# Kernel optimization log

Measured on AMD Instinct MI355X. Metric: run time of the kernel, lower is better.

The kernel has to match this reference:

```python
import jax, jax.numpy as jnp
import numpy as np

EPS = 1e-7  # K.epsilon()
SR = 10.0


def setup_inputs() -> dict:
    key = jax.random.key(0)
    ks = jax.random.split(key, 6)
    B, T, D, U = 32, 1024, 512, 64
    x1 = jax.random.normal(ks[0], (B, T, D), jnp.float32)
    x2 = jax.random.normal(ks[1], (B, T, D), jnp.float32)
    w1 = jax.random.normal(ks[2], (D, U), jnp.float32) * (2.0 / (D + U)) ** 0.5
    w2 = jax.random.normal(ks[3], (T, U), jnp.float32) * (2.0 / (T + U)) ** 0.5
    w3 = jax.random.normal(ks[4], (T, U), jnp.float32) * (2.0 / (T + U)) ** 0.5
    we = jax.random.normal(ks[5], (U, 1), jnp.float32) * (2.0 / (U + 1)) ** 0.5
    return {"x1": x1, "x2": x2, "w1": w1, "w2": w2, "w3": w3, "we": we}


def _branch(xa, xb, w1, w2, w3, we):
    # ab = xa @ xb^T over feature axis: (B,T,T); aa = xa @ xa^T
    ab = jnp.einsum('btd,bsd->bts', xa, xb)
    aa = jnp.einsum('btd,bsd->bts', xa, xa)
    # hidden: (B,T,U) -> score (B,T,1)
    h = jnp.tanh(jnp.einsum('bts,su->btu', ab, w2)
                 + jnp.einsum('bts,su->btu', aa, w3)
                 + jnp.einsum('btd,du->btu', xa, w1))
    eij = (h @ we) * SR  # (B,T,1)
    ai = jnp.exp(eij)
    ww = ai / (jnp.sum(ai, axis=1, keepdims=True) + EPS)
    return xa * ww  # (B,T,D)


def reference(x1, x2, w1, w2, w3, we):
    ot1 = _branch(x1, x2, w1, w2, w3, we)
    ot2 = _branch(x2, x1, w1, w2, w3, we)
    return (ot1, ot2)
```

## Files before the change

### kernel.cpp

```cpp
#include <hip/hip_runtime.h>
#include <math.h>

#define B_ 32
#define T_ 1024
#define D_ 512
#define U_ 64
#define TS_ 4
#define TH_ (T_/TS_)
#define TC_ 32
#define SR_ 10.0f
#define EPS_ 1e-7f

typedef __attribute__((ext_vector_type(8))) short bf16x8;
typedef __attribute__((ext_vector_type(4))) float f32x4;

#define LSTRIDE 40

__global__ __launch_bounds__(256, 3) void k1_partials(
    const float* __restrict__ x1, const float* __restrict__ x2,
    const float* __restrict__ w2, const float* __restrict__ w3,
    float* __restrict__ P)
{
    __shared__ ushort lds[8][64*LSTRIDE];

    const int dt  = blockIdx.x;
    const int ts  = blockIdx.y;
    const int b   = blockIdx.z;
    const int d0  = dt * 64;
    const int tid = threadIdx.x;
    const int lane = tid & 63;
    const int wid  = tid >> 6;
    const int wd   = wid & 1;
    const int wu   = wid >> 1;
    const int lr   = lane & 15;
    const int lg   = lane >> 4;
    const int col  = tid & 63;
    const int tq   = tid >> 6;

    f32x4 acc1[2][2], acc2[2][2];
    const f32x4 z = {0.f, 0.f, 0.f, 0.f};
    #pragma unroll
    for (int mi = 0; mi < 2; ++mi)
        #pragma unroll
        for (int ni = 0; ni < 2; ++ni) { acc1[mi][ni] = z; acc2[mi][ni] = z; }

    const size_t xb = (size_t)b * T_ * D_;

    for (int c = 0; c < TH_/TC_; ++c) {
        const int tb = ts*TH_ + c*TC_ + 8*tq;
        const float* ga[4] = { x1 + xb + (size_t)tb*D_ + d0 + col,
                               x2 + xb + (size_t)tb*D_ + d0 + col,
                               w2 + (size_t)tb*U_ + col,
                               w3 + (size_t)tb*U_ + col };
        const int stra[4] = { D_, D_, U_, U_ };
        #pragma unroll
        for (int a = 0; a < 4; ++a) {
            float v[8];
            #pragma unroll
            for (int j = 0; j < 8; ++j) v[j] = ga[a][(size_t)j * stra[a]];
            uint* hb = (uint*)lds[a*2];
            uint* lb = (uint*)lds[a*2+1];
            #pragma unroll
            for (int p = 0; p < 4; ++p) {
                float e = v[2*p], o = v[2*p+1];
                uint ue = __float_as_uint(e), uo = __float_as_uint(o);
                uint he = ue & 0xffff0000u, ho = uo & 0xffff0000u;
                float le = e - __uint_as_float(he);
                float lo = o - __uint_as_float(ho);
                int idx = col*(LSTRIDE/2) + 4*tq + p;
                hb[idx] = (he >> 16) | ho;
                lb[idx] = (__float_as_uint(le) >> 16) | (__float_as_uint(lo) & 0xffff0000u);
            }
        }
        __syncthreads();
        bf16x8 A1h[2], A1l[2], A2h[2], A2l[2];
        bf16x8 B2h[2], B2l[2], B3h[2], B3l[2];
        #pragma unroll
        for (int mi = 0; mi < 2; ++mi) {
            int off = (32*wd + 16*mi + lr)*LSTRIDE + 8*lg;
            A1h[mi] = *(const bf16x8*)&lds[0][off];
            A1l[mi] = *(const bf16x8*)&lds[1][off];
            A2h[mi] = *(const bf16x8*)&lds[2][off];
            A2l[mi] = *(const bf16x8*)&lds[3][off];
        }
        #pragma unroll
        for (int ni = 0; ni < 2; ++ni) {
            int off = (32*wu + 16*ni + lr)*LSTRIDE + 8*lg;
            B2h[ni] = *(const bf16x8*)&lds[4][off];
            B2l[ni] = *(const bf16x8*)&lds[5][off];
            B3h[ni] = *(const bf16x8*)&lds[6][off];
            B3l[ni] = *(const bf16x8*)&lds[7][off];
        }
        #pragma unroll
        for (int mi = 0; mi < 2; ++mi)
            #pragma unroll
            for (int ni = 0; ni < 2; ++ni) {
                f32x4 c1 = acc1[mi][ni];
                f32x4 c2 = acc2[mi][ni];
                c1 = __builtin_amdgcn_mfma_f32_16x16x32_bf16(A1h[mi], B3h[ni], c1, 0, 0, 0);
                c1 = __builtin_amdgcn_mfma_f32_16x16x32_bf16(A1h[mi], B3l[ni], c1, 0, 0, 0);
                c1 = __builtin_amdgcn_mfma_f32_16x16x32_bf16(A1l[mi], B3h[ni], c1, 0, 0, 0);
                c1 = __builtin_amdgcn_mfma_f32_16x16x32_bf16(A2h[mi], B2h[ni], c1, 0, 0, 0);
                c1 = __builtin_amdgcn_mfma_f32_16x16x32_bf16(A2h[mi], B2l[ni], c1, 0, 0, 0);
                c1 = __builtin_amdgcn_mfma_f32_16x16x32_bf16(A2l[mi], B2h[ni], c1, 0, 0, 0);
                c2 = __builtin_amdgcn_mfma_f32_16x16x32_bf16(A1h[mi], B2h[ni], c2, 0, 0, 0);
                c2 = __builtin_amdgcn_mfma_f32_16x16x32_bf16(A1h[mi], B2l[ni], c2, 0, 0, 0);
                c2 = __builtin_amdgcn_mfma_f32_16x16x32_bf16(A1l[mi], B2h[ni], c2, 0, 0, 0);
                c2 = __builtin_amdgcn_mfma_f32_16x16x32_bf16(A2h[mi], B3h[ni], c2, 0, 0, 0);
                c2 = __builtin_amdgcn_mfma_f32_16x16x32_bf16(A2h[mi], B3l[ni], c2, 0, 0, 0);
                c2 = __builtin_amdgcn_mfma_f32_16x16x32_bf16(A2l[mi], B3h[ni], c2, 0, 0, 0);
                acc1[mi][ni] = c1;
                acc2[mi][ni] = c2;
            }
        __syncthreads();
    }

    const size_t DU = (size_t)D_ * U_;
    const size_t base0 = (((size_t)ts*B_ + b)*2)*DU;
    #pragma unroll
    for (int mi = 0; mi < 2; ++mi)
        #pragma unroll
        for (int ni = 0; ni < 2; ++ni) {
            const int d = d0 + 32*wd + 16*mi + 4*lg;
            const int u = 32*wu + 16*ni + lr;
            #pragma unroll
            for (int r = 0; r < 4; ++r) {
                P[base0 + (size_t)(d+r)*U_ + u]      = acc1[mi][ni][r];
                P[base0 + DU + (size_t)(d+r)*U_ + u] = acc2[mi][ni][r];
            }
        }
}

__global__ __launch_bounds__(256) void k1_combine(
    const float* __restrict__ P, const float* __restrict__ w1,
    float* __restrict__ M1, float* __restrict__ M2)
{
    const int n = blockIdx.x*256 + threadIdx.x;
    const int b = n >> 13;
    const int r = n & 8191;
    const size_t du = (size_t)r * 4;
    const size_t DU = (size_t)D_ * U_;
    float4 w = *(const float4*)&w1[du];
    float4 s1 = w, s2 = w;
    #pragma unroll
    for (int ts = 0; ts < TS_; ++ts) {
        const float* Pb = P + (((size_t)ts*B_ + b)*2)*DU + du;
        float4 a = *(const float4*)&Pb[0];
        float4 c = *(const float4*)&Pb[DU];
        s1.x += a.x; s1.y += a.y; s1.z += a.z; s1.w += a.w;
        s2.x += c.x; s2.y += c.y; s2.z += c.z; s2.w += c.w;
    }
    *(float4*)&M1[(size_t)b*DU + du] = s1;
    *(float4*)&M2[(size_t)b*DU + du] = s2;
}

#define TT_ 64
#define XPAD_ 69
__global__ __launch_bounds__(256, 4) void k2_eij(
    const float* __restrict__ x1, const float* __restrict__ x2,
    const float* __restrict__ M1, const float* __restrict__ M2,
    const float* __restrict__ we, float* __restrict__ eij)
{
    __shared__ float xT[64*XPAD_];
    __shared__ float Ms[64*64];
    __shared__ float wes[64];
    __shared__ float red[16*TT_];

    const int tt = blockIdx.x;
    const int b  = blockIdx.y;
    const int br = blockIdx.z;
    const float* x = br ? x2 : x1;
    const float* M = (br ? M2 : M1) + (size_t)b * D_ * U_;
    const int tid = threadIdx.x;
    const int tdl = tid & 15;
    const int tu  = tid >> 4;
    if (tid < 64) wes[tid] = we[tid];

    float acc[4][4];
    #pragma unroll
    for (int i = 0; i < 4; ++i)
        #pragma unroll
        for (int j = 0; j < 4; ++j) acc[i][j] = 0.f;

    const size_t xb = (size_t)b*T_*D_ + (size_t)tt*TT_*D_;

    for (int c = 0; c < D_/64; ++c) {
        #pragma unroll
        for (int j = 0; j < 4; ++j) {
            int l  = j*256 + tid;
            int tl = l >> 4;
            int f  = (l & 15) << 2;
            float4 v = *(const float4*)&x[xb + (size_t)tl*D_ + c*64 + f];
            xT[(f+0)*XPAD_ + tl] = v.x;
            xT[(f+1)*XPAD_ + tl] = v.y;
            xT[(f+2)*XPAD_ + tl] = v.z;
            xT[(f+3)*XPAD_ + tl] = v.w;
        }
        #pragma unroll
        for (int j = 0; j < 4; ++j) {
            int l  = j*256 + tid;
            int dl = l >> 4;
            int f  = (l & 15) << 2;
            *(float4*)&Ms[dl*64 + f] = *(const float4*)&M[(size_t)(c*64 + dl)*U_ + f];
        }
        __syncthreads();
        #pragma unroll 4
        for (int d = 0; d < 64; ++d) {
            float4 xv = *(const float4*)&xT[d*XPAD_ + tdl*4];
            float4 mv = *(const float4*)&Ms[d*64 + tu*4];
            float xvv[4] = {xv.x,xv.y,xv.z,xv.w};
            float mvv[4] = {mv.x,mv.y,mv.z,mv.w};
            #pragma unroll
            for (int i = 0; i < 4; ++i)
                #pragma unroll
                for (int j = 0; j < 4; ++j)
                    acc[i][j] += xvv[i]*mvv[j];
        }
        __syncthreads();
    }

    #pragma unroll
    for (int i = 0; i < 4; ++i) {
        float p = 0.f;
        #pragma unroll
        for (int j = 0; j < 4; ++j)
            p += tanhf(acc[i][j]) * wes[tu*4 + j];
        red[tu*TT_ + tdl*4 + i] = p;
    }
    __syncthreads();
    if (tid < TT_) {
        float s = 0.f;
        #pragma unroll
        for (int q = 0; q < 16; ++q) s += red[q*TT_ + tid];
        eij[((size_t)br*B_ + b)*T_ + tt*TT_ + tid] = SR_ * s;
    }
}

__global__ __launch_bounds__(256) void k45_scale(
    const float* __restrict__ x1, const float* __restrict__ x2,
    const float* __restrict__ eij, float* __restrict__ out)
{
    __shared__ float sdata[256];
    __shared__ float wws[T_];

    const int tt = blockIdx.x;
    const int b  = blockIdx.y;
    const int br = blockIdx.z;
    const int tid = threadIdx.x;
    const float* e = eij + ((size_t)br*B_ + b) * T_;

    float v[4];
    float m = -1e30f;
    #pragma unroll
    for (int i = 0; i < 4; ++i) { v[i] = e[tid + i*256]; m = fmaxf(m, v[i]); }
    sdata[tid] = m; __syncthreads();
    for (int s = 128; s > 0; s >>= 1) {
        if (tid < s) sdata[tid] = fmaxf(sdata[tid], sdata[tid+s]);
        __syncthreads();
    }
    m = sdata[0]; __syncthreads();
    float ssum = 0.f;
    #pragma unroll
    for (int i = 0; i < 4; ++i) { v[i] = expf(v[i] - m); ssum += v[i]; }
    sdata[tid] = ssum; __syncthreads();
    for (int s = 128; s > 0; s >>= 1) {
        if (tid < s) sdata[tid] += sdata[tid+s];
        __syncthreads();
    }
    const float inv = 1.0f / (sdata[0] + EPS_ * expf(-m));
    #pragma unroll
    for (int i = 0; i < 4; ++i) wws[tid + i*256] = v[i] * inv;
    __syncthreads();

    const float* x = br ? x2 : x1;
    const size_t xb4 = ((size_t)b*T_ + (size_t)tt*64) * (D_/4);
    float* o = out + (size_t)br*B_*T_*D_;
    #pragma unroll
    for (int k = 0; k < 32; ++k) {
        int idx = k*256 + tid;
        int tl  = idx >> 7;
        float w = wws[tt*64 + tl];
        float4 xv = ((const float4*)x)[xb4 + idx];
        float4 ov = {xv.x*w, xv.y*w, xv.z*w, xv.w*w};
        ((float4*)o)[xb4 + idx] = ov;
    }
}

extern "C" void kernel_launch(void* const* d_in, const int* in_sizes, int n_in,
                              void* d_out, int out_size, void* d_ws, size_t ws_size,
                              hipStream_t stream)
{
    const float* x1 = (const float*)d_in[0];
    const float* x2 = (const float*)d_in[1];
    const float* w1 = (const float*)d_in[2];
    const float* w2 = (const float*)d_in[3];
    const float* w3 = (const float*)d_in[4];
    const float* we = (const float*)d_in[5];
    float* out = (float*)d_out;
    float* ws  = (float*)d_ws;

    float* P   = ws;
    float* M1  = P   + (size_t)TS_*B_*2*D_*U_;
    float* M2  = M1  + (size_t)B_*D_*U_;
    float* eij = M2  + (size_t)B_*D_*U_;

    k1_partials<<<dim3(8, TS_, B_), 256, 0, stream>>>(x1, x2, w2, w3, P);
    k1_combine <<<dim3((B_*D_*U_/4 + 255)/256), 256, 0, stream>>>(P, w1, M1, M2);
    k2_eij     <<<dim3(T_/TT_, B_, 2), 256, 0, stream>>>(x1, x2, M1, M2, we, eij);
    k45_scale  <<<dim3(16, B_, 2), 256, 0, stream>>>(x1, x2, eij, out);
}
```

Before: 373.4 us.

## Move k2 eij projection onto bf16x3 split MFMA with swizzled LDS

k2_eij now splits x and M into bf16 hi/lo halves and stores them in XOR-swizzled shared memory. It computes the x·M projection with 16x16x32 bf16 MFMA instructions, using three products (hh, hl, lh) to approximate fp32 accuracy, in place of the scalar fp32 FMA outer-product loop. The tanh·we reduction is now done with wave shuffles instead of a shared-memory reduction buffer. This trades extra conversion work and a small precision loss (the dropped lo·lo term) for much higher matrix throughput. The edits to k1 are cosmetic only.

```diff
diff --git a/kernel.cpp b/kernel.cpp
--- a/kernel.cpp
+++ b/kernel.cpp
@@ -8,6 +8,7 @@
 #define TS_ 4
 #define TH_ (T_/TS_)
 #define TC_ 32
+#define TT_ 64
 #define SR_ 10.0f
 #define EPS_ 1e-7f
 
@@ -15,6 +16,13 @@
 typedef __attribute__((ext_vector_type(4))) float f32x4;
 
 #define LSTRIDE 40
+
+__device__ __forceinline__ uint pack_hi2(float e, float o) {
+    return (__float_as_uint(e) >> 16) | (__float_as_uint(o) & 0xffff0000u);
+}
+__device__ __forceinline__ float hi_part(float v) {
+    return __uint_as_float(__float_as_uint(v) & 0xffff0000u);
+}
 
 __global__ __launch_bounds__(256, 3) void k1_partials(
     const float* __restrict__ x1, const float* __restrict__ x2,
@@ -63,8 +71,8 @@
             #pragma unroll
             for (int p = 0; p < 4; ++p) {
                 float e = v[2*p], o = v[2*p+1];
-                uint ue = __float_as_uint(e), uo = __float_as_uint(o);
-                uint he = ue & 0xffff0000u, ho = uo & 0xffff0000u;
+                uint he = __float_as_uint(e) & 0xffff0000u;
+                uint ho = __float_as_uint(o) & 0xffff0000u;
                 float le = e - __uint_as_float(he);
                 float lo = o - __uint_as_float(ho);
                 int idx = col*(LSTRIDE/2) + 4*tq + p;
@@ -154,85 +162,110 @@
     *(float4*)&M2[(size_t)b*DU + du] = s2;
 }
 
-#define TT_ 64
-#define XPAD_ 69
 __global__ __launch_bounds__(256, 4) void k2_eij(
     const float* __restrict__ x1, const float* __restrict__ x2,
     const float* __restrict__ M1, const float* __restrict__ M2,
     const float* __restrict__ we, float* __restrict__ eij)
 {
-    __shared__ float xT[64*XPAD_];
-    __shared__ float Ms[64*64];
-    __shared__ float wes[64];
-    __shared__ float red[16*TT_];
+    __shared__ ushort xh[64*64];
+    __shared__ ushort xl[64*64];
+    __shared__ ushort mh[64*64];
+    __shared__ ushort ml[64*64];
 
     const int tt = blockIdx.x;
     const int b  = blockIdx.y;
     const int br = blockIdx.z;
     const float* x = br ? x2 : x1;
     const float* M = (br ? M2 : M1) + (size_t)b * D_ * U_;
-    const int tid = threadIdx.x;
-    const int tdl = tid & 15;
-    const int tu  = tid >> 4;
-    if (tid < 64) wes[tid] = we[tid];
-
-    float acc[4][4];
-    #pragma unroll
-    for (int i = 0; i < 4; ++i)
-        #pragma unroll
-        for (int j = 0; j < 4; ++j) acc[i][j] = 0.f;
-
-    const size_t xb = (size_t)b*T_*D_ + (size_t)tt*TT_*D_;
+    const int tid  = threadIdx.x;
+    const int lane = tid & 63;
+    const int wid  = tid >> 6;
+    const int lr   = lane & 15;
+    const int lg   = lane >> 4;
+
+    const int s_tl = tid >> 4;
+    const int s_f4 = tid & 15;
+    const int m_u  = tid & 63;
+    const int m_dq = tid >> 6;
+
+    f32x4 acc[4];
+    const f32x4 z = {0.f, 0.f, 0.f, 0.f};
+    #pragma unroll
+    for (int ni = 0; ni < 4; ++ni) acc[ni] = z;
+
+    float wreg[4];
+    #pragma unroll
+    for (int ni = 0; ni < 4; ++ni) wreg[ni] = we[ni*16 + lr];
+
+    const size_t xbase = ((size_t)b*T_ + (size_t)tt*64) * D_;
 
     for (int c = 0; c < D_/64; ++c) {
+        const int d0 = c*64;
         #pragma unroll
         for (int j = 0; j < 4; ++j) {
-            int l  = j*256 + tid;
-            int tl = l >> 4;
-            int f  = (l & 15) << 2;
-            float4 v = *(const float4*)&x[xb + (size_t)tl*D_ + c*64 + f];
-            xT[(f+0)*XPAD_ + tl] = v.x;
-            xT[(f+1)*XPAD_ + tl] = v.y;
-            xT[(f+2)*XPAD_ + tl] = v.z;
-            xT[(f+3)*XPAD_ + tl] = v.w;
-        }
-        #pragma unroll
-        for (int j = 0; j < 4; ++j) {
-            int l  = j*256 + tid;
-            int dl = l >> 4;
-            int f  = (l & 15) << 2;
-            *(float4*)&Ms[dl*64 + f] = *(const float4*)&M[(size_t)(c*64 + dl)*U_ + f];
-        }
-        __syncthreads();
-        #pragma unroll 4
-        for (int d = 0; d < 64; ++d) {
-            float4 xv = *(const float4*)&xT[d*XPAD_ + tdl*4];
-            float4 mv = *(const float4*)&Ms[d*64 + tu*4];
-            float xvv[4] = {xv.x,xv.y,xv.z,xv.w};
-            float mvv[4] = {mv.x,mv.y,mv.z,mv.w};
-            #pragma unroll
-            for (int i = 0; i < 4; ++i)
-                #pragma unroll
-                for (int j = 0; j < 4; ++j)
-                    acc[i][j] += xvv[i]*mvv[j];
-        }
-        __syncthreads();
-    }
-
-    #pragma unroll
-    for (int i = 0; i < 4; ++i) {
-        float p = 0.f;
-        #pragma unroll
-        for (int j = 0; j < 4; ++j)
-            p += tanhf(acc[i][j]) * wes[tu*4 + j];
-        red[tu*TT_ + tdl*4 + i] = p;
-    }
-    __syncthreads();
-    if (tid < TT_) {
+            int t = j*16 + s_tl;
+            float4 v = *(const float4*)&x[xbase + (size_t)t*D_ + d0 + s_f4*4];
+            float hx = hi_part(v.x), hy = hi_part(v.y), hz = hi_part(v.z), hw = hi_part(v.w);
+            uint h0 = pack_hi2(v.x, v.y), h1 = pack_hi2(v.z, v.w);
+            uint l0 = pack_hi2(v.x - hx, v.y - hy);
+            uint l1 = pack_hi2(v.z - hz, v.w - hw);
+            int cu  = s_f4*2;
+            int swz = (t & 7) << 2;
+            ((uint*)xh)[t*32 + ((cu  ) ^ swz)] = h0;
+            ((uint*)xh)[t*32 + ((cu+1) ^ swz)] = h1;
+            ((uint*)xl)[t*32 + ((cu  ) ^ swz)] = l0;
+            ((uint*)xl)[t*32 + ((cu+1) ^ swz)] = l1;
+        }
+        {
+            int swz = (m_u & 7) << 2;
+            #pragma unroll
+            for (int j2 = 0; j2 < 8; ++j2) {
+                float e = M[(size_t)(d0 + m_dq*16 + 2*j2    )*U_ + m_u];
+                float o = M[(size_t)(d0 + m_dq*16 + 2*j2 + 1)*U_ + m_u];
+                float he = hi_part(e), ho = hi_part(o);
+                uint hm = pack_hi2(e, o);
+                uint lm = pack_hi2(e - he, o - ho);
+                int cu = m_dq*8 + j2;
+                ((uint*)mh)[m_u*32 + (cu ^ swz)] = hm;
+                ((uint*)ml)[m_u*32 + (cu ^ swz)] = lm;
+            }
+        }
+        __syncthreads();
+        #pragma unroll
+        for (int kk = 0; kk < 2; ++kk) {
+            const int ar   = wid*16 + lr;
+            const int aoff = ar*64 + (((lg + 4*kk)*8) ^ ((ar & 7) << 3));
+            bf16x8 Ah = *(const bf16x8*)&xh[aoff];
+            bf16x8 Al = *(const bf16x8*)&xl[aoff];
+            #pragma unroll
+            for (int ni = 0; ni < 4; ++ni) {
+                const int bu   = ni*16 + lr;
+                const int boff = bu*64 + (((lg + 4*kk)*8) ^ ((bu & 7) << 3));
+                bf16x8 Bh = *(const bf16x8*)&mh[boff];
+                bf16x8 Bl = *(const bf16x8*)&ml[boff];
+                f32x4 a = acc[ni];
+                a = __builtin_amdgcn_mfma_f32_16x16x32_bf16(Ah, Bh, a, 0, 0, 0);
+                a = __builtin_amdgcn_mfma_f32_16x16x32_bf16(Ah, Bl, a, 0, 0, 0);
+                a = __builtin_amdgcn_mfma_f32_16x16x32_bf16(Al, Bh, a, 0, 0, 0);
+                acc[ni] = a;
+            }
+        }
+        __syncthreads();
+    }
+
+    #pragma unroll
+    for (int r = 0; r < 4; ++r) {
         float s = 0.f;
         #pragma unroll
-        for (int q = 0; q < 16; ++q) s += red[q*TT_ + tid];
-        eij[((size_t)br*B_ + b)*T_ + tt*TT_ + tid] = SR_ * s;
+        for (int ni = 0; ni < 4; ++ni) s += tanhf(acc[ni][r]) * wreg[ni];
+        s += __shfl_xor(s, 1);
+        s += __shfl_xor(s, 2);
+        s += __shfl_xor(s, 4);
+        s += __shfl_xor(s, 8);
+        if (lr == 0) {
+            int t = tt*64 + wid*16 + lg*4 + r;
+            eij[((size_t)br*B_ + b)*T_ + t] = SR_ * s;
+        }
     }
 }
 
```

New measurement: 317.4 us. 15.0% less time.
